# Performance work log

Hardware: AMD Instinct MI355X
Metric: run time of the kernel (lower is better)

The kernel has to match this reference:

```python
import jax, jax.numpy as jnp
import numpy as np

N = 2048      # factor dims (d_in == units == N)
K = 16        # nonzeros per row of each factor
B = 16384     # batch
F = 3         # number of sparse factors
NNZ = N * K


def _pattern(f):
    # Fixed, compile-time-known structured sparsity pattern (butterfly-like):
    # row r has nonzeros at cols (r + k*(N//K) + f) % N, k in [0, K)
    r = np.repeat(np.arange(N), K)
    k = np.tile(np.arange(K), N)
    c = (r + k * (N // K) + f) % N
    return r.astype(np.int32), c.astype(np.int32)


def setup_inputs() -> dict:
    key = jax.random.key(0)
    kx, k0, k1, k2, ks, kb = jax.random.split(key, 6)
    # glorot-ish scale for sparse factor values: fan ~ K nonzeros per row
    wscale = (2.0 / (K + K)) ** 0.5
    rows0, cols0 = _pattern(0)
    rows1, cols1 = _pattern(1)
    rows2, cols2 = _pattern(2)
    return {
        "x": jax.random.normal(kx, (B, N), dtype=jnp.float32),
        "vals0": jax.random.normal(k0, (NNZ,), dtype=jnp.float32) * wscale,
        "vals1": jax.random.normal(k1, (NNZ,), dtype=jnp.float32) * wscale,
        "vals2": jax.random.normal(k2, (NNZ,), dtype=jnp.float32) * wscale,
        "rows0": jnp.asarray(rows0), "cols0": jnp.asarray(cols0),
        "rows1": jnp.asarray(rows1), "cols1": jnp.asarray(cols1),
        "rows2": jnp.asarray(rows2), "cols2": jnp.asarray(cols2),
        "scaling": jax.random.uniform(ks, (1,), dtype=jnp.float32, minval=0.5, maxval=1.5),
        "bias": jax.random.normal(kb, (N,), dtype=jnp.float32) * 0.02,
    }


def _dense_factor(vals, rows, cols):
    # materialize the sparse factor (values scattered into the fixed pattern)
    return jnp.zeros((N, N), dtype=vals.dtype).at[rows, cols].set(vals)


def reference(x, vals0, vals1, vals2, rows0, cols0, rows1, cols1, rows2, cols2, scaling, bias):
    # output = relu(scaling * (x @ W0 @ W1 @ W2) + bias)
    y = x
    for vals, rows, cols in ((vals0, rows0, cols0), (vals1, rows1, cols1), (vals2, rows2, cols2)):
        y = y @ _dense_factor(vals, rows, cols)  # [B, N]
    y = scaling * y + bias
    return jax.nn.relu(y)
```

## Files before the change

kernel.cpp:

```cpp
#include <hip/hip_runtime.h>

#define NN 2048
#define KK 16

__global__ __launch_bounds__(256) void sfd_compose01(const float* __restrict__ v0,
                                                     const float* __restrict__ v1,
                                                     float* __restrict__ w01) {
  int tid = blockIdx.x * 256 + threadIdx.x;
  int c1 = tid >> 4;
  int i  = tid & 15;
  int cm = (c1 + NN - 1) & (NN - 1);
  int s1 = cm & 127;
  int t1 = cm >> 7;
  int rx = s1 + (i << 7);
  float acc = 0.f;
#pragma unroll
  for (int k1 = 0; k1 < 16; ++k1) {
    int r0 = (cm - (k1 << 7)) & (NN - 1);
    int k0 = (t1 - k1 - i) & 15;
    acc = fmaf(v1[r0 * 16 + k1], v0[rx * 16 + k0], acc);
  }
  w01[c1 * 16 + i] = acc;
}

__global__ __launch_bounds__(256) void sfd_compose012(const float* __restrict__ v2,
                                                      const float* __restrict__ w01,
                                                      const float* __restrict__ scaling,
                                                      float* __restrict__ mcl) {
  int tid = blockIdx.x * 256 + threadIdx.x;
  int c = tid >> 4;
  int i = tid & 15;
  float acc = 0.f;
#pragma unroll
  for (int k2 = 0; k2 < 16; ++k2) {
    int r1 = (c + NN - 2 - (k2 << 7)) & (NN - 1);
    acc = fmaf(v2[r1 * 16 + k2], w01[r1 * 16 + i], acc);
  }
  int s = c & 127;
  int j = c >> 7;
  mcl[(s * 16 + j) * 16 + i] = acc * scaling[0];
}

__global__ __launch_bounds__(256, 8) void sfd_apply(const float* __restrict__ x,
                                                    const float* __restrict__ mcl,
                                                    const float* __restrict__ bias,
                                                    float* __restrict__ out) {
  const int S0 = blockIdx.x << 5;
  const int b0 = blockIdx.y << 5;
  const int t = threadIdx.x;
  const int u = t & 31;
  const int jp = t >> 5;
  const int s = S0 + u;
  const int j0 = jp << 1;
  const int w0 = (S0 + 125) & 127;
  const int shift = (w0 + u) >> 7;

  float mc0[16], mc1[16];
  {
    const float* r0p = mcl + ((s * 16 + j0) << 4);
#pragma unroll
    for (int i = 0; i < 16; ++i) {
      int ic = (i + shift) & 15;
      mc0[i] = r0p[ic];
      mc1[i] = r0p[16 + ic];
    }
  }
  const int c0 = s + (j0 << 7);
  const int c1 = c0 + 128;
  const float bi0 = bias[c0];
  const float bi1 = bias[c1];

  __shared__ float xs[8 * 32 * 20];

  for (int ch = 0; ch < 4; ++ch) {
    const int rb = b0 + (ch << 3);
#pragma unroll
    for (int q = 0; q < 4; ++q) {
      int idx = t + (q << 8);
      int uu = idx & 31;
      int ig = (idx >> 5) & 3;
      int rr = idx >> 7;
      const float* xrow = x + (size_t)(rb + rr) * NN;
      int cb = w0 + uu + (ig << 9);
      float4 v;
      v.x = xrow[cb & (NN - 1)];
      v.y = xrow[(cb + 128) & (NN - 1)];
      v.z = xrow[(cb + 256) & (NN - 1)];
      v.w = xrow[(cb + 384) & (NN - 1)];
      *(float4*)(xs + (rr * 32 + uu) * 20 + (ig << 2)) = v;
    }
    __syncthreads();
#pragma unroll 1
    for (int r = 0; r < 8; ++r) {
      const float4* xr = (const float4*)(xs + (r * 32 + u) * 20);
      float xv[16];
      *(float4*)(xv + 0)  = xr[0];
      *(float4*)(xv + 4)  = xr[1];
      *(float4*)(xv + 8)  = xr[2];
      *(float4*)(xv + 12) = xr[3];
      float acc0 = bi0, acc1 = bi1;
#pragma unroll
      for (int i = 0; i < 16; ++i) {
        acc0 = fmaf(xv[i], mc0[i], acc0);
        acc1 = fmaf(xv[i], mc1[i], acc1);
      }
      size_t ob = (size_t)(rb + r) * NN;
      __builtin_nontemporal_store(fmaxf(acc0, 0.f), &out[ob + c0]);
      __builtin_nontemporal_store(fmaxf(acc1, 0.f), &out[ob + c1]);
    }
    __syncthreads();
  }
}

extern "C" void kernel_launch(void* const* d_in, const int* in_sizes, int n_in,
                              void* d_out, int out_size, void* d_ws, size_t ws_size,
                              hipStream_t stream) {
  const float* x       = (const float*)d_in[0];
  const float* v0      = (const float*)d_in[1];
  const float* v1      = (const float*)d_in[2];
  const float* v2      = (const float*)d_in[3];
  const float* scaling = (const float*)d_in[10];
  const float* bias    = (const float*)d_in[11];
  float* out = (float*)d_out;

  float* w01 = (float*)d_ws;
  float* mcl = w01 + NN * KK;

  const int B = in_sizes[0] / NN;

  hipLaunchKernelGGL(sfd_compose01, dim3(128), dim3(256), 0, stream, v0, v1, w01);
  hipLaunchKernelGGL(sfd_compose012, dim3(128), dim3(256), 0, stream, v2, w01, scaling, mcl);
  hipLaunchKernelGGL(sfd_apply, dim3(4, B >> 5), dim3(256), 0, stream, x, mcl, bias, out);
}
```

Before: 272.5 us.

## Replace shared-memory staging with register double-buffered direct global loads

The apply kernel no longer stages x tiles through LDS with block barriers. Each thread instead loads its 16 strided x values straight into registers, prefetching the next row while computing the current one. The coefficient rotation is removed by computing wrapped column offsets directly, and the occupancy hint is lowered to allow more registers. The aim is to remove LDS round trips and barrier stalls while hiding load latency. The cost is higher register pressure and lower occupancy.

```diff
diff --git a/kernel.cpp b/kernel.cpp
--- a/kernel.cpp
+++ b/kernel.cpp
@@ -41,7 +41,7 @@
   mcl[(s * 16 + j) * 16 + i] = acc * scaling[0];
 }
 
-__global__ __launch_bounds__(256, 8) void sfd_apply(const float* __restrict__ x,
+__global__ __launch_bounds__(256, 4) void sfd_apply(const float* __restrict__ x,
                                                     const float* __restrict__ mcl,
                                                     const float* __restrict__ bias,
                                                     float* __restrict__ out) {
@@ -53,62 +53,59 @@
   const int s = S0 + u;
   const int j0 = jp << 1;
   const int w0 = (S0 + 125) & 127;
-  const int shift = (w0 + u) >> 7;
+  const int res = (w0 + u) & 127;
 
   float mc0[16], mc1[16];
   {
     const float* r0p = mcl + ((s * 16 + j0) << 4);
 #pragma unroll
-    for (int i = 0; i < 16; ++i) {
-      int ic = (i + shift) & 15;
-      mc0[i] = r0p[ic];
-      mc1[i] = r0p[16 + ic];
-    }
+    for (int i = 0; i < 16; ++i) { mc0[i] = r0p[i]; mc1[i] = r0p[16 + i]; }
   }
+
+  int off[16];
+#pragma unroll
+  for (int i = 0; i < 16; ++i) off[i] = res + (i << 7);
+
   const int c0 = s + (j0 << 7);
   const int c1 = c0 + 128;
   const float bi0 = bias[c0];
   const float bi1 = bias[c1];
 
-  __shared__ float xs[8 * 32 * 20];
+  const float* xr0 = x + (size_t)b0 * NN;
+  float xa[16], xb[16];
+#pragma unroll
+  for (int i = 0; i < 16; ++i) xa[i] = xr0[off[i]];
 
-  for (int ch = 0; ch < 4; ++ch) {
-    const int rb = b0 + (ch << 3);
+  for (int r = 0; r < 32; r += 2) {
+    const float* xcur = x + (size_t)(b0 + r) * NN;
 #pragma unroll
-    for (int q = 0; q < 4; ++q) {
-      int idx = t + (q << 8);
-      int uu = idx & 31;
-      int ig = (idx >> 5) & 3;
-      int rr = idx >> 7;
-      const float* xrow = x + (size_t)(rb + rr) * NN;
-      int cb = w0 + uu + (ig << 9);
-      float4 v;
-      v.x = xrow[cb & (NN - 1)];
-      v.y = xrow[(cb + 128) & (NN - 1)];
-      v.z = xrow[(cb + 256) & (NN - 1)];
-      v.w = xrow[(cb + 384) & (NN - 1)];
-      *(float4*)(xs + (rr * 32 + uu) * 20 + (ig << 2)) = v;
-    }
-    __syncthreads();
-#pragma unroll 1
-    for (int r = 0; r < 8; ++r) {
-      const float4* xr = (const float4*)(xs + (r * 32 + u) * 20);
-      float xv[16];
-      *(float4*)(xv + 0)  = xr[0];
-      *(float4*)(xv + 4)  = xr[1];
-      *(float4*)(xv + 8)  = xr[2];
-      *(float4*)(xv + 12) = xr[3];
+    for (int i = 0; i < 16; ++i) xb[i] = xcur[NN + off[i]];
+    {
       float acc0 = bi0, acc1 = bi1;
 #pragma unroll
       for (int i = 0; i < 16; ++i) {
-        acc0 = fmaf(xv[i], mc0[i], acc0);
-        acc1 = fmaf(xv[i], mc1[i], acc1);
+        acc0 = fmaf(xa[i], mc0[i], acc0);
+        acc1 = fmaf(xa[i], mc1[i], acc1);
       }
-      size_t ob = (size_t)(rb + r) * NN;
+      size_t ob = (size_t)(b0 + r) * NN;
       __builtin_nontemporal_store(fmaxf(acc0, 0.f), &out[ob + c0]);
       __builtin_nontemporal_store(fmaxf(acc1, 0.f), &out[ob + c1]);
     }
-    __syncthreads();
+    if (r + 2 < 32) {
+#pragma unroll
+      for (int i = 0; i < 16; ++i) xa[i] = xcur[2 * NN + off[i]];
+    }
+    {
+      float acc0 = bi0, acc1 = bi1;
+#pragma unroll
+      for (int i = 0; i < 16; ++i) {
+        acc0 = fmaf(xb[i], mc0[i], acc0);
+        acc1 = fmaf(xb[i], mc1[i], acc1);
+      }
+      size_t ob = (size_t)(b0 + r + 1) * NN;
+      __builtin_nontemporal_store(fmaxf(acc0, 0.f), &out[ob + c0]);
+      __builtin_nontemporal_store(fmaxf(acc1, 0.f), &out[ob + c1]);
+    }
   }
 }
 
```

Measured after the change: 303.5 us. 11.4% more time.
